# Performance work log

Hardware: AMD Instinct MI355X
Metric: run time of the kernel (lower is better)

## Reference

```python
import jax, jax.numpy as jnp
import numpy as np

INPUT_SIZE, HIDDEN_SIZE, OUTPUT_SIZE, NUM_LAYERS = 64, 128, 32, 2
B, T = 256, 1024


def setup_inputs() -> dict:
    key = jax.random.key(0)
    ks = jax.random.split(key, 12)
    s = 1.0 / np.sqrt(HIDDEN_SIZE)  # PyTorch LSTM init range
    x = jax.random.normal(ks[0], (B, T, INPUT_SIZE), dtype=jnp.float32)
    h0 = jnp.zeros((NUM_LAYERS, B, HIDDEN_SIZE), dtype=jnp.float32)
    c0 = jnp.zeros((NUM_LAYERS, B, HIDDEN_SIZE), dtype=jnp.float32)
    # layer 0: input -> hidden; layer 1: hidden -> hidden. Gate order i,f,g,o (PyTorch).
    W_ih0 = jax.random.uniform(ks[1], (4 * HIDDEN_SIZE, INPUT_SIZE), minval=-s, maxval=s)
    W_hh0 = jax.random.uniform(ks[2], (4 * HIDDEN_SIZE, HIDDEN_SIZE), minval=-s, maxval=s)
    b_ih0 = jax.random.uniform(ks[3], (4 * HIDDEN_SIZE,), minval=-s, maxval=s)
    b_hh0 = jax.random.uniform(ks[4], (4 * HIDDEN_SIZE,), minval=-s, maxval=s)
    W_ih1 = jax.random.uniform(ks[5], (4 * HIDDEN_SIZE, HIDDEN_SIZE), minval=-s, maxval=s)
    W_hh1 = jax.random.uniform(ks[6], (4 * HIDDEN_SIZE, HIDDEN_SIZE), minval=-s, maxval=s)
    b_ih1 = jax.random.uniform(ks[7], (4 * HIDDEN_SIZE,), minval=-s, maxval=s)
    b_hh1 = jax.random.uniform(ks[8], (4 * HIDDEN_SIZE,), minval=-s, maxval=s)
    fc_w = jax.random.uniform(ks[9], (OUTPUT_SIZE, HIDDEN_SIZE), minval=-s, maxval=s)
    fc_b = jax.random.uniform(ks[10], (OUTPUT_SIZE,), minval=-s, maxval=s)
    return dict(x=x, h0=h0, c0=c0,
                W_ih0=W_ih0, W_hh0=W_hh0, b_ih0=b_ih0, b_hh0=b_hh0,
                W_ih1=W_ih1, W_hh1=W_hh1, b_ih1=b_ih1, b_hh1=b_hh1,
                fc_w=fc_w, fc_b=fc_b)


def _lstm_layer(x_btf, h0, c0, W_ih, W_hh, b_ih, b_hh):
    """x_btf: [B,T,F] -> (out [B,T,H], hT [B,H], cT [B,H]). PyTorch gate order i,f,g,o."""
    H = h0.shape[-1]
    # Precompute input contribution for all timesteps as one big GEMM.
    xp = jnp.einsum('btf,gf->btg', x_btf, W_ih) + b_ih + b_hh  # [B,T,4H]
    xp = jnp.swapaxes(xp, 0, 1)  # time-major [T,B,4H]

    def step(carry, xp_t):
        h, c = carry
        gates = xp_t + h @ W_hh.T  # [B,4H]
        i = jax.nn.sigmoid(gates[:, 0 * H:1 * H])
        f = jax.nn.sigmoid(gates[:, 1 * H:2 * H])
        g = jnp.tanh(gates[:, 2 * H:3 * H])
        o = jax.nn.sigmoid(gates[:, 3 * H:4 * H])
        c = f * c + i * g
        h = o * jnp.tanh(c)
        return (h, c), h

    (hT, cT), hs = jax.lax.scan(step, (h0, c0), xp)
    return jnp.swapaxes(hs, 0, 1), hT, cT  # back to batch_first


def reference(x, h0, c0, W_ih0, W_hh0, b_ih0, b_hh0,
              W_ih1, W_hh1, b_ih1, b_hh1, fc_w, fc_b):
    out0, h_0, c_0 = _lstm_layer(x, h0[0], c0[0], W_ih0, W_hh0, b_ih0, b_hh0)
    out1, h_1, c_1 = _lstm_layer(out0, h0[1], c0[1], W_ih1, W_hh1, b_ih1, b_hh1)
    out = jnp.einsum('bth,oh->bto', out1, fc_w) + fc_b  # [B,T,output_size]
    hN = jnp.stack([h_0, h_1])  # [num_layers,B,H]
    cN = jnp.stack([c_0, c_1])
    return out, hN, cN
```

## Files before the change

kernel.cpp:

```cpp
#include <hip/hip_runtime.h>


static constexpr int B   = 256;
static constexpr int T   = 1024;
static constexpr int H   = 128;
static constexpr int O   = 32;
static constexpr int R   = 4;
static constexpr int NBL = B / R;
static constexpr int CH  = 8;
static constexpr int NCH = T / CH;

static constexpr int HROW = H + 8;
static constexpr int HB   = 0;
static constexpr int HH   = HB + 2 * 16 * HROW;
static constexpr int XROW = 72;
static constexpr int XB   = HH + 2 * 16 * HROW;
static constexpr int LDSN = XB + 2 * 32 * XROW;

typedef __attribute__((ext_vector_type(8))) short  short8;
typedef __attribute__((ext_vector_type(4))) float  f32x4;

#define LOG2E 1.4426950408889634f

#if __has_builtin(__builtin_amdgcn_exp2f)
#define EXP2(x) __builtin_amdgcn_exp2f(x)
#else
#define EXP2(x) __expf((x) * 0.69314718056f)
#endif
#if __has_builtin(__builtin_amdgcn_rcpf)
#define RCP(x) __builtin_amdgcn_rcpf(x)
#else
#define RCP(x) (1.0f / (x))
#endif

__device__ __forceinline__ unsigned short f2bf(float f) {
  unsigned int u = __builtin_bit_cast(unsigned int, f);
  u += 0x7fffu + ((u >> 16) & 1u);
  return (unsigned short)(u >> 16);
}

__device__ __forceinline__ float sigm(float x) {
  return RCP(1.0f + EXP2(-LOG2E * x));
}
__device__ __forceinline__ float tanh_f(float x) {
  return 1.0f - 2.0f * RCP(1.0f + EXP2(2.0f * LOG2E * x));
}

__device__ __forceinline__ short8 cvt8(const float* s) {
  float4 a = *(const float4*)s;
  float4 b = *(const float4*)(s + 4);
  short8 v;
  v[0] = (short)f2bf(a.x); v[1] = (short)f2bf(a.y);
  v[2] = (short)f2bf(a.z); v[3] = (short)f2bf(a.w);
  v[4] = (short)f2bf(b.x); v[5] = (short)f2bf(b.y);
  v[6] = (short)f2bf(b.z); v[7] = (short)f2bf(b.w);
  return v;
}

__device__ __forceinline__ void block_sync_lds() {
  __builtin_amdgcn_sched_barrier(0);
  asm volatile("s_waitcnt lgkmcnt(0)" ::: "memory");
  __builtin_amdgcn_s_barrier();
  __builtin_amdgcn_sched_barrier(0);
}

template <int KIN, bool IN_BF16, bool WRITE_HOUT, bool FUSE_FC, bool PROD, bool CONS>
__device__ __forceinline__ void scan_body(
    unsigned short* __restrict__ S,
    const void* __restrict__ in_,
    const float* __restrict__ h0,
    const float* __restrict__ c0,
    const float* __restrict__ Wih,
    const float* __restrict__ Whh,
    const float* __restrict__ bih,
    const float* __restrict__ bhh,
    unsigned short* __restrict__ hout,
    float* __restrict__ hN,
    float* __restrict__ cN,
    const float* __restrict__ Wfc,
    const float* __restrict__ bfc,
    float* __restrict__ fco,
    int* __restrict__ flag, const int bbase)
{
  constexpr int KCX = KIN / 32;
  constexpr int KCH = H / 32;

  const int tid  = threadIdx.x;
  const int w    = tid >> 6;
  const int l    = tid & 63;
  const int l15  = l & 15;
  const int lhi  = l >> 4;
  const int jcol = w * 16 + l15;

  short8 wfh[4][KCH], wfx[4][KCX];
  float  bias4[4];
#pragma unroll
  for (int gb = 0; gb < 4; ++gb) {
    const int gc = gb * H + jcol;
#pragma unroll
    for (int kc = 0; kc < KCX; ++kc)
      wfx[gb][kc] = cvt8(Wih + (size_t)gc * KIN + kc * 32 + lhi * 8);
#pragma unroll
    for (int kc = 0; kc < KCH; ++kc)
      wfh[gb][kc] = cvt8(Whh + (size_t)gc * H + kc * 32 + lhi * 8);
    bias4[gb] = bih[gc] + bhh[gc];
  }

  short8 bfr[4];
  float fcbias = 0.f;
  if constexpr (FUSE_FC) {
    const int oc = (w & 1) * 16 + l15;
#pragma unroll
    for (int kc = 0; kc < 4; ++kc)
      bfr[kc] = cvt8(Wfc + (size_t)oc * H + kc * 32 + lhi * 8);
    fcbias = bfc[oc];
  }

  float cst   = c0[(size_t)(bbase + lhi) * H + jcol];
  float hlast = 0.f;

  const float*          inf = (const float*)in_;
  const unsigned short* inb = (const unsigned short*)in_;

  const int srow = tid >> 4;
  const int scol = (tid & 15) * 4;
  const float* xs0 = inf +
      ((size_t)(bbase + ((srow & 15) >> 2)) * T + ((srow >> 4) * 4 + (srow & 3))) * KIN + scol;

  const unsigned short* xg1 =
      inb + ((size_t)(bbase + (l15 >> 2)) * T + (l15 & 3)) * KIN + lhi * 8;

  unsigned short* hp = nullptr;
  if constexpr (WRITE_HOUT)
    hp = hout + (size_t)(bbase + lhi) * T * H + jcol;

  for (int i = tid; i < 2 * 16 * HROW / 2; i += 512)
    ((unsigned int*)S)[i] = 0u;

  if constexpr (CONS) {
    if (tid == 0) {
      while (__hip_atomic_load(flag, __ATOMIC_ACQUIRE, __HIP_MEMORY_SCOPE_AGENT) < 2)
        __builtin_amdgcn_s_sleep(4);
    }
  }
  __syncthreads();

  S[HB + (lhi * 4) * HROW + jcol] = f2bf(h0[(size_t)(bbase + lhi) * H + jcol]);
  short8 xfr[2][KCX];
  if constexpr (!IN_BF16) {
    float4 v = *(const float4*)xs0;
    uint2 p;
    p.x = (unsigned int)f2bf(v.x) | ((unsigned int)f2bf(v.y) << 16);
    p.y = (unsigned int)f2bf(v.z) | ((unsigned int)f2bf(v.w) << 16);
    *(uint2*)&S[XB + srow * XROW + scol] = p;
  } else {
#pragma unroll
    for (int q = 0; q < 2; ++q)
#pragma unroll
      for (int kc = 0; kc < KCX; ++kc)
        xfr[q][kc] = *(const short8*)(xg1 + (size_t)(q * 4) * KIN + kc * 32);
  }
  __syncthreads();

  for (int k = 0; k < NCH; ++k) {
    if constexpr (CONS) {
      if (k > 0) {
        const int want = (k + 2 > NCH) ? NCH : (k + 2);
        if (tid == 0) {
          while (__hip_atomic_load(flag, __ATOMIC_ACQUIRE, __HIP_MEMORY_SCOPE_AGENT) < want)
            __builtin_amdgcn_s_sleep(4);
        }
        __syncthreads();
      }
    }

    const bool hasN = (k + 1 < NCH);

    f32x4 axc2[4][2];
#pragma unroll
    for (int q = 0; q < 2; ++q) {
      short8 afx[KCX];
#pragma unroll
      for (int kc = 0; kc < KCX; ++kc) {
        if constexpr (IN_BF16)
          afx[kc] = xfr[q][kc];
        else
          afx[kc] = *(const short8*)&S[XB + ((k & 1) * 32 + q * 16 + l15) * XROW +
                                       kc * 32 + lhi * 8];
      }
#pragma unroll
      for (int gb = 0; gb < 4; ++gb) {
        f32x4 a = {bias4[gb], bias4[gb], bias4[gb], bias4[gb]};
#pragma unroll
        for (int kc = 0; kc < KCX; ++kc)
          a = __builtin_amdgcn_mfma_f32_16x16x32_bf16(afx[kc], wfx[gb][kc], a, 0, 0, 0);
        axc2[gb][q] = a;
      }
    }

    float4 pf;
#pragma unroll
    for (int tt = 0; tt < CH; ++tt) {
      const int cur = tt & 1, nxt = cur ^ 1;

      if constexpr (!IN_BF16) {
        if (tt == 0 && hasN) pf = *(const float4*)(xs0 + (size_t)(k + 1) * CH * KIN);
        if (tt == 1 && hasN) {
          uint2 p;
          p.x = (unsigned int)f2bf(pf.x) | ((unsigned int)f2bf(pf.y) << 16);
          p.y = (unsigned int)f2bf(pf.z) | ((unsigned int)f2bf(pf.w) << 16);
          *(uint2*)&S[XB + (((k + 1) & 1) * 32 + srow) * XROW + scol] = p;
        }
      } else {
        if (tt == 0 && hasN) {
#pragma unroll
          for (int q = 0; q < 2; ++q)
#pragma unroll
            for (int kc = 0; kc < KCX; ++kc)
              xfr[q][kc] = *(const short8*)(
                  xg1 + (size_t)((k + 1) * CH + q * 4) * KIN + kc * 32);
        }
      }

      short8 afh[KCH];
#pragma unroll
      for (int kc = 0; kc < KCH; ++kc)
        afh[kc] = *(const short8*)&S[HB + (cur * 16 + l15) * HROW + kc * 32 + lhi * 8];

      f32x4 acc[4];
#pragma unroll
      for (int gb = 0; gb < 4; ++gb) {
        const float ax = axc2[gb][tt >> 2][tt & 3];
        f32x4 a = {ax, ax, ax, ax};
#pragma unroll
        for (int kc = 0; kc < KCH; ++kc)
          a = __builtin_amdgcn_mfma_f32_16x16x32_bf16(afh[kc], wfh[gb][kc], a, 0, 0, 0);
        acc[gb] = a;
      }

      {
        float i_ = sigm(acc[0][0]);
        float f_ = sigm(acc[1][0]);
        float g_ = tanh_f(acc[2][0]);
        float o_ = sigm(acc[3][0]);
        float c_ = f_ * cst + i_ * g_;
        cst = c_;
        float hn = o_ * tanh_f(c_);
        hlast = hn;
        unsigned short hb = f2bf(hn);
        S[HB + (nxt * 16 + lhi * 4) * HROW + jcol] = hb;
        if constexpr (FUSE_FC)
          S[HH + ((lhi >> 1) * 16 + (lhi & 1) * 8 + tt) * HROW + jcol] = hb;
        if constexpr (WRITE_HOUT) { hp[0] = hb; hp += H; }
      }

      block_sync_lds();
    }

    if constexpr (FUSE_FC) {
      if (w < 4) {
        const int q = w >> 1;
        short8 a4[4];
#pragma unroll
        for (int kc = 0; kc < 4; ++kc)
          a4[kc] = *(const short8*)&S[HH + (q * 16 + l15) * HROW + kc * 32 + lhi * 8];
        f32x4 fs = {fcbias, fcbias, fcbias, fcbias};
#pragma unroll
        for (int kc = 0; kc < 4; ++kc)
          fs = __builtin_amdgcn_mfma_f32_16x16x32_bf16(a4[kc], bfr[kc], fs, 0, 0, 0);
        const int brow = bbase + q * 2 + (lhi >> 1);
        const int tb   = k * CH + (lhi & 1) * 4;
#pragma unroll
        for (int r = 0; r < 4; ++r)
          fco[((size_t)brow * T + tb + r) * O + (w & 1) * 16 + l15] = fs[r];
      }
    }

    if constexpr (PROD) {
      __builtin_amdgcn_sched_barrier(0);
      asm volatile("s_waitcnt vmcnt(0)" ::: "memory");
      __builtin_amdgcn_s_barrier();
      if (tid == 0)
        __hip_atomic_store(flag, k + 1, __ATOMIC_RELEASE, __HIP_MEMORY_SCOPE_AGENT);
    }
  }

  hN[(size_t)(bbase + lhi) * H + jcol] = hlast;
  cN[(size_t)(bbase + lhi) * H + jcol] = cst;
}

__global__ __launch_bounds__(512, 2) void lstm_fused(
    const float* __restrict__ x,
    const float* __restrict__ h0, const float* __restrict__ c0,
    const float* __restrict__ Wih0, const float* __restrict__ Whh0,
    const float* __restrict__ bih0, const float* __restrict__ bhh0,
    const float* __restrict__ Wih1, const float* __restrict__ Whh1,
    const float* __restrict__ bih1, const float* __restrict__ bhh1,
    const float* __restrict__ fcw, const float* __restrict__ fcb,
    unsigned short* __restrict__ out0,
    float* __restrict__ out, float* __restrict__ hN, float* __restrict__ cN,
    int* __restrict__ flags)
{
  __shared__ __align__(16) unsigned short S[LDSN];
  const int bid = blockIdx.x;
  if (bid < NBL) {
    scan_body<64, false, true, false, true, false>(
        S, x, h0, c0, Wih0, Whh0, bih0, bhh0,
        out0, hN, cN, nullptr, nullptr, nullptr,
        flags + bid, bid * R);
  } else {
    const int rb = bid - NBL;
    scan_body<128, true, false, true, false, true>(
        S, out0, h0 + B * H, c0 + B * H, Wih1, Whh1, bih1, bhh1,
        nullptr, hN + B * H, cN + B * H, fcw, fcb, out,
        flags + rb, rb * R);
  }
}

extern "C" void kernel_launch(void* const* d_in, const int* in_sizes, int n_in,
                              void* d_out, int out_size, void* d_ws, size_t ws_size,
                              hipStream_t stream) {
  (void)in_sizes; (void)n_in; (void)out_size; (void)ws_size;

  const float* x    = (const float*)d_in[0];
  const float* h0   = (const float*)d_in[1];
  const float* c0   = (const float*)d_in[2];
  const float* Wih0 = (const float*)d_in[3];
  const float* Whh0 = (const float*)d_in[4];
  const float* bih0 = (const float*)d_in[5];
  const float* bhh0 = (const float*)d_in[6];
  const float* Wih1 = (const float*)d_in[7];
  const float* Whh1 = (const float*)d_in[8];
  const float* bih1 = (const float*)d_in[9];
  const float* bhh1 = (const float*)d_in[10];
  const float* fcw  = (const float*)d_in[11];
  const float* fcb  = (const float*)d_in[12];

  int*            flags = (int*)d_ws;
  unsigned short* out0  = (unsigned short*)((char*)d_ws + 1024);

  float* out = (float*)d_out;
  float* hN  = out + (size_t)B * T * O;
  float* cN  = hN + (size_t)2 * B * H;

  hipMemsetAsync(d_ws, 0, 1024, stream);
  lstm_fused<<<2 * NBL, 512, 0, stream>>>(
      x, h0, c0, Wih0, Whh0, bih0, bhh0, Wih1, Whh1, bih1, bhh1,
      fcw, fcb, out0, out, hN, cN, flags);
}
```

Before: 746.9 us.

## Software-pipeline next chunk's input projection into recurrent timesteps

Moves the per-chunk input-projection MFMAs out of the chunk prologue and spreads them across timesteps 2-5 of the previous chunk. They now overlap with the serial recurrent step instead of stalling before it. The change also halves the bf16 input prefetch register buffer by loading it in two halves, and reloads FC weights inside the FC block each chunk to free registers. The cost is extra per-chunk global loads for FC weights and more complex scheduling on the latency-critical recurrence path.

```diff
diff --git a/kernel.cpp b/kernel.cpp
--- a/kernel.cpp
+++ b/kernel.cpp
@@ -106,16 +106,6 @@
     bias4[gb] = bih[gc] + bhh[gc];
   }
 
-  short8 bfr[4];
-  float fcbias = 0.f;
-  if constexpr (FUSE_FC) {
-    const int oc = (w & 1) * 16 + l15;
-#pragma unroll
-    for (int kc = 0; kc < 4; ++kc)
-      bfr[kc] = cvt8(Wfc + (size_t)oc * H + kc * 32 + lhi * 8);
-    fcbias = bfc[oc];
-  }
-
   float cst   = c0[(size_t)(bbase + lhi) * H + jcol];
   float hlast = 0.f;
 
@@ -146,21 +136,36 @@
   __syncthreads();
 
   S[HB + (lhi * 4) * HROW + jcol] = f2bf(h0[(size_t)(bbase + lhi) * H + jcol]);
-  short8 xfr[2][KCX];
   if constexpr (!IN_BF16) {
     float4 v = *(const float4*)xs0;
     uint2 p;
     p.x = (unsigned int)f2bf(v.x) | ((unsigned int)f2bf(v.y) << 16);
     p.y = (unsigned int)f2bf(v.z) | ((unsigned int)f2bf(v.w) << 16);
     *(uint2*)&S[XB + srow * XROW + scol] = p;
-  } else {
-#pragma unroll
-    for (int q = 0; q < 2; ++q)
+  }
+  __syncthreads();
+
+  f32x4 axc2[4][2];
+  short8 xfr[KCX];
+#pragma unroll
+  for (int q = 0; q < 2; ++q) {
+    short8 afx[KCX];
+#pragma unroll
+    for (int kc = 0; kc < KCX; ++kc) {
+      if constexpr (IN_BF16)
+        afx[kc] = *(const short8*)(xg1 + (size_t)(q * 4) * KIN + kc * 32);
+      else
+        afx[kc] = *(const short8*)&S[XB + (q * 16 + l15) * XROW + kc * 32 + lhi * 8];
+    }
+#pragma unroll
+    for (int gb = 0; gb < 4; ++gb) {
+      f32x4 a = {bias4[gb], bias4[gb], bias4[gb], bias4[gb]};
 #pragma unroll
       for (int kc = 0; kc < KCX; ++kc)
-        xfr[q][kc] = *(const short8*)(xg1 + (size_t)(q * 4) * KIN + kc * 32);
-  }
-  __syncthreads();
+        a = __builtin_amdgcn_mfma_f32_16x16x32_bf16(afx[kc], wfx[gb][kc], a, 0, 0, 0);
+      axc2[gb][q] = a;
+    }
+  }
 
   for (int k = 0; k < NCH; ++k) {
     if constexpr (CONS) {
@@ -175,30 +180,9 @@
     }
 
     const bool hasN = (k + 1 < NCH);
-
-    f32x4 axc2[4][2];
-#pragma unroll
-    for (int q = 0; q < 2; ++q) {
-      short8 afx[KCX];
-#pragma unroll
-      for (int kc = 0; kc < KCX; ++kc) {
-        if constexpr (IN_BF16)
-          afx[kc] = xfr[q][kc];
-        else
-          afx[kc] = *(const short8*)&S[XB + ((k & 1) * 32 + q * 16 + l15) * XROW +
-                                       kc * 32 + lhi * 8];
-      }
-#pragma unroll
-      for (int gb = 0; gb < 4; ++gb) {
-        f32x4 a = {bias4[gb], bias4[gb], bias4[gb], bias4[gb]};
-#pragma unroll
-        for (int kc = 0; kc < KCX; ++kc)
-          a = __builtin_amdgcn_mfma_f32_16x16x32_bf16(afx[kc], wfx[gb][kc], a, 0, 0, 0);
-        axc2[gb][q] = a;
-      }
-    }
-
+    f32x4 axn[4][2];
     float4 pf;
+
 #pragma unroll
     for (int tt = 0; tt < CH; ++tt) {
       const int cur = tt & 1, nxt = cur ^ 1;
@@ -214,11 +198,8 @@
       } else {
         if (tt == 0 && hasN) {
 #pragma unroll
-          for (int q = 0; q < 2; ++q)
-#pragma unroll
-            for (int kc = 0; kc < KCX; ++kc)
-              xfr[q][kc] = *(const short8*)(
-                  xg1 + (size_t)((k + 1) * CH + q * 4) * KIN + kc * 32);
+          for (int kc = 0; kc < KCX; ++kc)
+            xfr[kc] = *(const short8*)(xg1 + (size_t)((k + 1) * CH) * KIN + kc * 32);
         }
       }
 
@@ -236,16 +217,47 @@
         for (int kc = 0; kc < KCH; ++kc)
           a = __builtin_amdgcn_mfma_f32_16x16x32_bf16(afh[kc], wfh[gb][kc], a, 0, 0, 0);
         acc[gb] = a;
+      }
+
+      if (hasN && tt >= 2 && tt <= 5) {
+        const int q  = (tt - 2) >> 1;
+        const int g0 = ((tt - 2) & 1) * 2;
+        short8 afx[KCX];
+#pragma unroll
+        for (int kc = 0; kc < KCX; ++kc) {
+          if constexpr (IN_BF16)
+            afx[kc] = xfr[kc];
+          else
+            afx[kc] = *(const short8*)&S[XB + (((k + 1) & 1) * 32 + q * 16 + l15) * XROW +
+                                         kc * 32 + lhi * 8];
+        }
+#pragma unroll
+        for (int gg = 0; gg < 2; ++gg) {
+          const int gb = g0 + gg;
+          f32x4 a = {bias4[gb], bias4[gb], bias4[gb], bias4[gb]};
+#pragma unroll
+          for (int kc = 0; kc < KCX; ++kc)
+            a = __builtin_amdgcn_mfma_f32_16x16x32_bf16(afx[kc], wfx[gb][kc], a, 0, 0, 0);
+          axn[gb][q] = a;
+        }
+      }
+      if constexpr (IN_BF16) {
+        if (tt == 3 && hasN) {
+#pragma unroll
+          for (int kc = 0; kc < KCX; ++kc)
+            xfr[kc] = *(const short8*)(xg1 + (size_t)((k + 1) * CH + 4) * KIN + kc * 32);
+        }
       }
 
       {
         float i_ = sigm(acc[0][0]);
         float f_ = sigm(acc[1][0]);
         float g_ = tanh_f(acc[2][0]);
-        float o_ = sigm(acc[3][0]);
         float c_ = f_ * cst + i_ * g_;
         cst = c_;
-        float hn = o_ * tanh_f(c_);
+        float tc = tanh_f(c_);
+        float o_ = sigm(acc[3][0]);
+        float hn = o_ * tc;
         hlast = hn;
         unsigned short hb = f2bf(hn);
         S[HB + (nxt * 16 + lhi * 4) * HROW + jcol] = hb;
@@ -259,12 +271,18 @@
 
     if constexpr (FUSE_FC) {
       if (w < 4) {
+        short8 bfr[4];
+        const int oc = (w & 1) * 16 + l15;
+#pragma unroll
+        for (int kc = 0; kc < 4; ++kc)
+          bfr[kc] = cvt8(Wfc + (size_t)oc * H + kc * 32 + lhi * 8);
+        const float fcb_ = bfc[oc];
         const int q = w >> 1;
         short8 a4[4];
 #pragma unroll
         for (int kc = 0; kc < 4; ++kc)
           a4[kc] = *(const short8*)&S[HH + (q * 16 + l15) * HROW + kc * 32 + lhi * 8];
-        f32x4 fs = {fcbias, fcbias, fcbias, fcbias};
+        f32x4 fs = {fcb_, fcb_, fcb_, fcb_};
 #pragma unroll
         for (int kc = 0; kc < 4; ++kc)
           fs = __builtin_amdgcn_mfma_f32_16x16x32_bf16(a4[kc], bfr[kc], fs, 0, 0, 0);
@@ -273,6 +291,14 @@
 #pragma unroll
         for (int r = 0; r < 4; ++r)
           fco[((size_t)brow * T + tb + r) * O + (w & 1) * 16 + l15] = fs[r];
+      }
+    }
+
+    if (hasN) {
+#pragma unroll
+      for (int gb = 0; gb < 4; ++gb) {
+        axc2[gb][0] = axn[gb][0];
+        axc2[gb][1] = axn[gb][1];
       }
     }
 
```

Result: slower. 2.495 ms (+234.0%).
